# Optimization experiments

Measured on AMD Instinct MI355X. Metric: run time of the kernel, lower is better.

## Reference

```python
import jax, jax.numpy as jnp
import numpy as np

N = 500_000   # total nodes across the batch of graphs
D = 256       # node feature dim
G = 4096      # number of graphs (segments)


def setup_inputs() -> dict:
    key = jax.random.key(0)
    k1, k2, k3 = jax.random.split(key, 3)
    x = jax.random.normal(k1, (N, D), dtype=jnp.float32)
    batch = jnp.sort(jax.random.randint(k2, (N,), 0, G, dtype=jnp.int64))
    Wg = jax.random.normal(k3, (D,), dtype=jnp.float32) * (1.0 / np.sqrt(D))
    bg = jnp.zeros((1,), dtype=jnp.float32)
    return {"x": x, "batch": batch, "Wg": Wg, "bg": bg}


def reference(x, batch, Wg, bg):
    # gate_nn: Linear(D, 1), then squeeze -> [N]
    gate = x @ Wg + bg[0]
    # scatter_softmax over segments defined by batch
    gmax = jax.ops.segment_max(gate, batch, num_segments=G, indices_are_sorted=True)
    e = jnp.exp(gate - gmax[batch])
    denom = jax.ops.segment_sum(e, batch, num_segments=G, indices_are_sorted=True)
    attn = e / denom[batch]
    # weighted scatter-add pooling -> [G, D]
    out = jax.ops.segment_sum(x * attn[:, None], batch, num_segments=G,
                              indices_are_sorted=True)
    return out
```

## Files before the change

kernel.cpp:

```cpp
#include <hip/hip_runtime.h>
#include <math.h>


#define DIM 256

__device__ __forceinline__ int lower_bound(const int* __restrict__ b, int n, int key) {
    int lo = 0, hi = n;
    while (lo < hi) {
        int mid = (lo + hi) >> 1;
        if (b[mid] < key) lo = mid + 1; else hi = mid;
    }
    return lo;
}

__global__ void build_offsets_kernel(const int* __restrict__ batch,
                                     int* __restrict__ offs, int N, int G) {
    int i = blockIdx.x * blockDim.x + threadIdx.x;
    const int stride = gridDim.x * blockDim.x;
    for (; i < N; i += stride) {
        const int b    = batch[i];
        const int prev = (i == 0) ? -1 : batch[i - 1];
        for (int g = prev + 1; g <= b; ++g) offs[g] = i;
        if (i == N - 1) {
            for (int g = b + 1; g <= G; ++g) offs[g] = N;
        }
    }
}

__device__ __forceinline__ float dot4(const float4 a, const float4 b) {
    return fmaf(a.x, b.x, fmaf(a.y, b.y, fmaf(a.z, b.z, a.w * b.w)));
}

__global__ __launch_bounds__(256)
void gap_fused_kernel(const float* __restrict__ x,
                      const int* __restrict__ batch,
                      const float* __restrict__ Wg,
                      const float* __restrict__ bg,
                      const int* __restrict__ offs,
                      float* __restrict__ out,
                      int N) {
    const int g    = blockIdx.x;
    const int tid  = threadIdx.x;
    const int lane = tid & 63;
    const int wv   = tid >> 6;

    int start, end;
    if (offs) {
        start = offs[g];
        end   = offs[g + 1];
    } else {
        start = lower_bound(batch, N, g);
        end   = lower_bound(batch, N, g + 1);
    }

    __shared__ float s_ml[8];
    __shared__ float s_acc[4 * DIM];

    if (start >= end) {
        out[(size_t)g * DIM + tid] = 0.0f;
        return;
    }

    const float4 wgv  = ((const float4*)Wg)[lane];
    const float  bias = bg[0];
    const int    len  = end - start;
    const float4* __restrict__ x4 = (const float4*)x + (size_t)start * (DIM / 4);

    float  m   = -INFINITY;
    float  l   = 0.0f;
    float4 acc = make_float4(0.f, 0.f, 0.f, 0.f);

    const int ntiles = (len + 15) >> 4;
    const int rb     = wv * 4;
    const int lmax   = len - 1;

    auto ridx = [&](int row) -> size_t {
        const int rr = row < lmax ? row : lmax;
        return (size_t)rr * 64 + lane;
    };

    float4 c0 = x4[ridx(rb + 0)];
    float4 c1 = x4[ridx(rb + 1)];
    float4 c2 = x4[ridx(rb + 2)];
    float4 c3 = x4[ridx(rb + 3)];

    for (int j = 0; j < ntiles; ++j) {
        const int base = j * 16 + rb;

        const int nb = base + 16;
        float4 n0 = x4[ridx(nb + 0)];
        float4 n1 = x4[ridx(nb + 1)];
        float4 n2 = x4[ridx(nb + 2)];
        float4 n3 = x4[ridx(nb + 3)];

        float d0 = dot4(c0, wgv);
        float d1 = dot4(c1, wgv);
        float d2 = dot4(c2, wgv);
        float d3 = dot4(c3, wgv);
        #pragma unroll
        for (int off = 32; off; off >>= 1) {
            d0 += __shfl_xor(d0, off);
            d1 += __shfl_xor(d1, off);
            d2 += __shfl_xor(d2, off);
            d3 += __shfl_xor(d3, off);
        }
        const bool v0 = (base + 0) < len;
        const bool v1 = (base + 1) < len;
        const bool v2 = (base + 2) < len;
        const bool v3 = (base + 3) < len;
        const float g0 = v0 ? d0 + bias : -INFINITY;
        const float g1 = v1 ? d1 + bias : -INFINITY;
        const float g2 = v2 ? d2 + bias : -INFINITY;
        const float g3 = v3 ? d3 + bias : -INFINITY;

        const float nm    = fmaxf(m, fmaxf(fmaxf(g0, g1), fmaxf(g2, g3)));
        const float alpha = (m == nm) ? 1.0f : __expf(m - nm);
        const float p0 = v0 ? __expf(g0 - nm) : 0.0f;
        const float p1 = v1 ? __expf(g1 - nm) : 0.0f;
        const float p2 = v2 ? __expf(g2 - nm) : 0.0f;
        const float p3 = v3 ? __expf(g3 - nm) : 0.0f;
        l = fmaf(l, alpha, (p0 + p1) + (p2 + p3));
        acc.x = fmaf(p0, c0.x, fmaf(p1, c1.x, fmaf(p2, c2.x, fmaf(p3, c3.x, acc.x * alpha))));
        acc.y = fmaf(p0, c0.y, fmaf(p1, c1.y, fmaf(p2, c2.y, fmaf(p3, c3.y, acc.y * alpha))));
        acc.z = fmaf(p0, c0.z, fmaf(p1, c1.z, fmaf(p2, c2.z, fmaf(p3, c3.z, acc.z * alpha))));
        acc.w = fmaf(p0, c0.w, fmaf(p1, c1.w, fmaf(p2, c2.w, fmaf(p3, c3.w, acc.w * alpha))));
        m = nm;

        c0 = n0; c1 = n1; c2 = n2; c3 = n3;
    }

    if (lane == 0) { s_ml[wv] = m; s_ml[4 + wv] = l; }
    ((float4*)s_acc)[wv * 64 + lane] = acc;
    __syncthreads();

    const float M = fmaxf(fmaxf(s_ml[0], s_ml[1]), fmaxf(s_ml[2], s_ml[3]));
    float denom = 0.f, val = 0.f;
    #pragma unroll
    for (int w = 0; w < 4; ++w) {
        const float sc = __expf(s_ml[w] - M);
        denom = fmaf(s_ml[4 + w], sc, denom);
        val   = fmaf(s_acc[w * DIM + tid], sc, val);
    }
    out[(size_t)g * DIM + tid] = val / denom;
}

extern "C" void kernel_launch(void* const* d_in, const int* in_sizes, int n_in,
                              void* d_out, int out_size, void* d_ws, size_t ws_size,
                              hipStream_t stream) {
    const float* x     = (const float*)d_in[0];
    const int*   batch = (const int*)d_in[1];
    const float* Wg    = (const float*)d_in[2];
    const float* bg    = (const float*)d_in[3];
    float*       out   = (float*)d_out;

    const int N = in_sizes[1];
    const int G = out_size / DIM;

    int* offs = nullptr;
    if (d_ws != nullptr && ws_size >= (size_t)(G + 1) * sizeof(int)) {
        offs = (int*)d_ws;
        build_offsets_kernel<<<1024, 256, 0, stream>>>(batch, offs, N, G);
    }
    gap_fused_kernel<<<G, DIM, 0, stream>>>(x, batch, Wg, bg, offs, out, N);
}
```

Before: 655.9 us.

## Deepen per-wave row batch to 8 with masked-free main loop and nontemporal loads

Each wave now processes 8 rows per iteration instead of 4, giving 32 rows per block tile and twice as many loads in flight for the software prefetch. Full tiles run without validity masks, and only a single tail tile is masked. Loads and the output store use nontemporal builtins to avoid polluting cache with streamed data, and launch bounds request 4 blocks per CU. The wider batch raises register pressure, and groups shorter than 32 rows now go entirely through the tail path, whose 8-row loads are clamped to the group's last row.

```diff
diff --git a/kernel.cpp b/kernel.cpp
--- a/kernel.cpp
+++ b/kernel.cpp
@@ -3,6 +3,8 @@
 
 
 #define DIM 256
+
+typedef float f32x4 __attribute__((ext_vector_type(4)));
 
 __device__ __forceinline__ int lower_bound(const int* __restrict__ b, int n, int key) {
     int lo = 0, hi = n;
@@ -27,11 +29,11 @@
     }
 }
 
-__device__ __forceinline__ float dot4(const float4 a, const float4 b) {
-    return fmaf(a.x, b.x, fmaf(a.y, b.y, fmaf(a.z, b.z, a.w * b.w)));
-}
-
-__global__ __launch_bounds__(256)
+__device__ __forceinline__ float dot4(const f32x4 a, const f32x4 b) {
+    return fmaf(a[0], b[0], fmaf(a[1], b[1], fmaf(a[2], b[2], a[3] * b[3])));
+}
+
+__global__ __launch_bounds__(256, 4)
 void gap_fused_kernel(const float* __restrict__ x,
                       const int* __restrict__ batch,
                       const float* __restrict__ Wg,
@@ -61,76 +63,131 @@
         return;
     }
 
-    const float4 wgv  = ((const float4*)Wg)[lane];
-    const float  bias = bg[0];
-    const int    len  = end - start;
-    const float4* __restrict__ x4 = (const float4*)x + (size_t)start * (DIM / 4);
-
-    float  m   = -INFINITY;
-    float  l   = 0.0f;
-    float4 acc = make_float4(0.f, 0.f, 0.f, 0.f);
-
-    const int ntiles = (len + 15) >> 4;
-    const int rb     = wv * 4;
-    const int lmax   = len - 1;
-
-    auto ridx = [&](int row) -> size_t {
+    const f32x4 wgv  = ((const f32x4*)Wg)[lane];
+    const float bias = bg[0];
+    const int   len  = end - start;
+    const int   lmax = len - 1;
+    const f32x4* __restrict__ xb =
+        (const f32x4*)x + (size_t)start * (DIM / 4) + lane;
+
+    auto ld = [&](int row) -> f32x4 {
         const int rr = row < lmax ? row : lmax;
-        return (size_t)rr * 64 + lane;
+        return __builtin_nontemporal_load(xb + (size_t)rr * (DIM / 4));
     };
 
-    float4 c0 = x4[ridx(rb + 0)];
-    float4 c1 = x4[ridx(rb + 1)];
-    float4 c2 = x4[ridx(rb + 2)];
-    float4 c3 = x4[ridx(rb + 3)];
-
-    for (int j = 0; j < ntiles; ++j) {
-        const int base = j * 16 + rb;
-
-        const int nb = base + 16;
-        float4 n0 = x4[ridx(nb + 0)];
-        float4 n1 = x4[ridx(nb + 1)];
-        float4 n2 = x4[ridx(nb + 2)];
-        float4 n3 = x4[ridx(nb + 3)];
-
-        float d0 = dot4(c0, wgv);
-        float d1 = dot4(c1, wgv);
-        float d2 = dot4(c2, wgv);
-        float d3 = dot4(c3, wgv);
+    float m = -INFINITY;
+    float l = 0.0f;
+    f32x4 acc = {0.f, 0.f, 0.f, 0.f};
+
+    const int rb    = wv * 8;
+    const int nfull = len >> 5;
+
+    f32x4 c0, c1, c2, c3, c4, c5, c6, c7;
+    bool have_c = false;
+
+    if (nfull > 0) {
+        c0 = ld(rb + 0); c1 = ld(rb + 1); c2 = ld(rb + 2); c3 = ld(rb + 3);
+        c4 = ld(rb + 4); c5 = ld(rb + 5); c6 = ld(rb + 6); c7 = ld(rb + 7);
+
+        for (int j = 0; j < nfull; ++j) {
+            const int nb = (j + 1) * 32 + rb;
+            f32x4 n0 = ld(nb + 0), n1 = ld(nb + 1), n2 = ld(nb + 2), n3 = ld(nb + 3);
+            f32x4 n4 = ld(nb + 4), n5 = ld(nb + 5), n6 = ld(nb + 6), n7 = ld(nb + 7);
+
+            float d0 = dot4(c0, wgv), d1 = dot4(c1, wgv), d2 = dot4(c2, wgv), d3 = dot4(c3, wgv);
+            float d4 = dot4(c4, wgv), d5 = dot4(c5, wgv), d6 = dot4(c6, wgv), d7 = dot4(c7, wgv);
+            #pragma unroll
+            for (int off = 32; off; off >>= 1) {
+                d0 += __shfl_xor(d0, off); d1 += __shfl_xor(d1, off);
+                d2 += __shfl_xor(d2, off); d3 += __shfl_xor(d3, off);
+                d4 += __shfl_xor(d4, off); d5 += __shfl_xor(d5, off);
+                d6 += __shfl_xor(d6, off); d7 += __shfl_xor(d7, off);
+            }
+            d0 += bias; d1 += bias; d2 += bias; d3 += bias;
+            d4 += bias; d5 += bias; d6 += bias; d7 += bias;
+
+            const float mx = fmaxf(fmaxf(fmaxf(d0, d1), fmaxf(d2, d3)),
+                                   fmaxf(fmaxf(d4, d5), fmaxf(d6, d7)));
+            const float nm    = fmaxf(m, mx);
+            const float alpha = __expf(m - nm);
+            const float p0 = __expf(d0 - nm), p1 = __expf(d1 - nm);
+            const float p2 = __expf(d2 - nm), p3 = __expf(d3 - nm);
+            const float p4 = __expf(d4 - nm), p5 = __expf(d5 - nm);
+            const float p6 = __expf(d6 - nm), p7 = __expf(d7 - nm);
+            l = fmaf(l, alpha, ((p0 + p1) + (p2 + p3)) + ((p4 + p5) + (p6 + p7)));
+            #pragma unroll
+            for (int k = 0; k < 4; ++k) {
+                float a = acc[k] * alpha;
+                a = fmaf(p0, c0[k], a); a = fmaf(p1, c1[k], a);
+                a = fmaf(p2, c2[k], a); a = fmaf(p3, c3[k], a);
+                a = fmaf(p4, c4[k], a); a = fmaf(p5, c5[k], a);
+                a = fmaf(p6, c6[k], a); a = fmaf(p7, c7[k], a);
+                acc[k] = a;
+            }
+            m = nm;
+
+            c0 = n0; c1 = n1; c2 = n2; c3 = n3;
+            c4 = n4; c5 = n5; c6 = n6; c7 = n7;
+        }
+        have_c = true;
+    }
+
+    const int trem = len - (nfull << 5);
+    if (trem > 0) {
+        const int base = (nfull << 5) + rb;
+        if (!have_c) {
+            c0 = ld(base + 0); c1 = ld(base + 1); c2 = ld(base + 2); c3 = ld(base + 3);
+            c4 = ld(base + 4); c5 = ld(base + 5); c6 = ld(base + 6); c7 = ld(base + 7);
+        }
+        float d0 = dot4(c0, wgv), d1 = dot4(c1, wgv), d2 = dot4(c2, wgv), d3 = dot4(c3, wgv);
+        float d4 = dot4(c4, wgv), d5 = dot4(c5, wgv), d6 = dot4(c6, wgv), d7 = dot4(c7, wgv);
         #pragma unroll
         for (int off = 32; off; off >>= 1) {
-            d0 += __shfl_xor(d0, off);
-            d1 += __shfl_xor(d1, off);
-            d2 += __shfl_xor(d2, off);
-            d3 += __shfl_xor(d3, off);
-        }
-        const bool v0 = (base + 0) < len;
-        const bool v1 = (base + 1) < len;
-        const bool v2 = (base + 2) < len;
-        const bool v3 = (base + 3) < len;
+            d0 += __shfl_xor(d0, off); d1 += __shfl_xor(d1, off);
+            d2 += __shfl_xor(d2, off); d3 += __shfl_xor(d3, off);
+            d4 += __shfl_xor(d4, off); d5 += __shfl_xor(d5, off);
+            d6 += __shfl_xor(d6, off); d7 += __shfl_xor(d7, off);
+        }
+        const bool v0 = (base + 0) < len, v1 = (base + 1) < len;
+        const bool v2 = (base + 2) < len, v3 = (base + 3) < len;
+        const bool v4 = (base + 4) < len, v5 = (base + 5) < len;
+        const bool v6 = (base + 6) < len, v7 = (base + 7) < len;
         const float g0 = v0 ? d0 + bias : -INFINITY;
         const float g1 = v1 ? d1 + bias : -INFINITY;
         const float g2 = v2 ? d2 + bias : -INFINITY;
         const float g3 = v3 ? d3 + bias : -INFINITY;
-
-        const float nm    = fmaxf(m, fmaxf(fmaxf(g0, g1), fmaxf(g2, g3)));
+        const float g4 = v4 ? d4 + bias : -INFINITY;
+        const float g5 = v5 ? d5 + bias : -INFINITY;
+        const float g6 = v6 ? d6 + bias : -INFINITY;
+        const float g7 = v7 ? d7 + bias : -INFINITY;
+
+        const float mx = fmaxf(fmaxf(fmaxf(g0, g1), fmaxf(g2, g3)),
+                               fmaxf(fmaxf(g4, g5), fmaxf(g6, g7)));
+        const float nm    = fmaxf(m, mx);
         const float alpha = (m == nm) ? 1.0f : __expf(m - nm);
         const float p0 = v0 ? __expf(g0 - nm) : 0.0f;
         const float p1 = v1 ? __expf(g1 - nm) : 0.0f;
         const float p2 = v2 ? __expf(g2 - nm) : 0.0f;
         const float p3 = v3 ? __expf(g3 - nm) : 0.0f;
-        l = fmaf(l, alpha, (p0 + p1) + (p2 + p3));
-        acc.x = fmaf(p0, c0.x, fmaf(p1, c1.x, fmaf(p2, c2.x, fmaf(p3, c3.x, acc.x * alpha))));
-        acc.y = fmaf(p0, c0.y, fmaf(p1, c1.y, fmaf(p2, c2.y, fmaf(p3, c3.y, acc.y * alpha))));
-        acc.z = fmaf(p0, c0.z, fmaf(p1, c1.z, fmaf(p2, c2.z, fmaf(p3, c3.z, acc.z * alpha))));
-        acc.w = fmaf(p0, c0.w, fmaf(p1, c1.w, fmaf(p2, c2.w, fmaf(p3, c3.w, acc.w * alpha))));
+        const float p4 = v4 ? __expf(g4 - nm) : 0.0f;
+        const float p5 = v5 ? __expf(g5 - nm) : 0.0f;
+        const float p6 = v6 ? __expf(g6 - nm) : 0.0f;
+        const float p7 = v7 ? __expf(g7 - nm) : 0.0f;
+        l = fmaf(l, alpha, ((p0 + p1) + (p2 + p3)) + ((p4 + p5) + (p6 + p7)));
+        #pragma unroll
+        for (int k = 0; k < 4; ++k) {
+            float a = acc[k] * alpha;
+            a = fmaf(p0, c0[k], a); a = fmaf(p1, c1[k], a);
+            a = fmaf(p2, c2[k], a); a = fmaf(p3, c3[k], a);
+            a = fmaf(p4, c4[k], a); a = fmaf(p5, c5[k], a);
+            a = fmaf(p6, c6[k], a); a = fmaf(p7, c7[k], a);
+            acc[k] = a;
+        }
         m = nm;
-
-        c0 = n0; c1 = n1; c2 = n2; c3 = n3;
     }
 
     if (lane == 0) { s_ml[wv] = m; s_ml[4 + wv] = l; }
-    ((float4*)s_acc)[wv * 64 + lane] = acc;
+    ((f32x4*)s_acc)[wv * 64 + lane] = acc;
     __syncthreads();
 
     const float M = fmaxf(fmaxf(s_ml[0], s_ml[1]), fmaxf(s_ml[2], s_ml[3]));
@@ -141,7 +198,7 @@
         denom = fmaf(s_ml[4 + w], sc, denom);
         val   = fmaf(s_acc[w * DIM + tid], sc, val);
     }
-    out[(size_t)g * DIM + tid] = val / denom;
+    __builtin_nontemporal_store(val / denom, &out[(size_t)g * DIM + tid]);
 }
 
 extern "C" void kernel_launch(void* const* d_in, const int* in_sizes, int n_in,
```

Result: faster. 620.3 us (-5.4%).
